# Performance work log

Hardware: AMD Instinct MI355X
Metric: run time of the kernel (lower is better)

The kernel has to match this reference:

```python
import jax, jax.numpy as jnp
import numpy as np

H = 1024  # hidden size

def _gru_layer(x, h0_l, w_ih_l, w_hh_l, b_ih_l, b_hh_l):
    # x: [T,B,I]; precompute input gates for all timesteps (like addmm in the kernel)
    x_gates = jnp.einsum('tbi,gi->tbg', x, w_ih_l) + b_ih_l  # [T,B,3H]

    def step(h, xg):
        # h: [B,H]; xg: [B,3H]
        h_gates = h @ w_hh_l.T + b_hh_l  # [B,3H]
        xr, xz, xn = xg[:, :H], xg[:, H:2*H], xg[:, 2*H:]
        hr, hz, hn = h_gates[:, :H], h_gates[:, H:2*H], h_gates[:, 2*H:]
        r = jax.nn.sigmoid(xr + hr)
        z = jax.nn.sigmoid(xz + hz)
        n = jnp.tanh(xn + r * hn)
        h_new = (1.0 - z) * n + z * h
        return h_new, h_new

    h_final, seq_out = jax.lax.scan(step, h0_l, x_gates)
    return h_final, seq_out


def setup_inputs() -> dict:
    key = jax.random.key(0)
    ks = jax.random.split(key, 6)
    T, B, I, L = 512, 64, 1024, 2
    s = 1.0 / np.sqrt(H)
    return {
        'x': jax.random.normal(ks[0], (T, B, I), dtype=jnp.float32),
        'h0': jax.random.normal(ks[1], (L, B, H), dtype=jnp.float32),
        'w_ih': jax.random.normal(ks[2], (L, 3 * H, I), dtype=jnp.float32) * s,
        'w_hh': jax.random.normal(ks[3], (L, 3 * H, H), dtype=jnp.float32) * s,
        'b_ih': jax.random.normal(ks[4], (L, 3 * H), dtype=jnp.float32) * s,
        'b_hh': jax.random.normal(ks[5], (L, 3 * H), dtype=jnp.float32) * s,
    }


def reference(x, h0, w_ih, w_hh, b_ih, b_hh):
    num_layers = h0.shape[0]
    h_n = []
    cur = x
    for l in range(num_layers):
        h_final, seq_out = _gru_layer(cur, h0[l], w_ih[l], w_hh[l], b_ih[l], b_hh[l])
        h_n.append(h_final)
        cur = seq_out  # layer output becomes next layer's input
    # kernel returns only the final hidden state of every layer, in fp32
    return jnp.stack(h_n, axis=0)  # [L,B,H]
```

## Files before the change

### kernel.cpp

```cpp
#include <hip/hip_runtime.h>

typedef unsigned short u16;
typedef unsigned long long u64;
typedef __attribute__((ext_vector_type(8))) short short8;
typedef __attribute__((ext_vector_type(4))) float f32x4;

#define HH 1024
#define BB 64
#define TT 512
#define G3 3072
#define NBLK 192
#define NS 513
#define SLOT (BB * HH)
#define FSTRIDE 32
#define RING 8

__device__ __forceinline__ u16 f2b(float f) {
  unsigned u = __float_as_uint(f);
  unsigned r = (u + 0x7fffu + ((u >> 16) & 1u)) >> 16;
  return (u16)r;
}
__device__ __forceinline__ float b2f(u16 h) {
  return __uint_as_float(((unsigned)h) << 16);
}
__device__ __forceinline__ float ftanh(float x) {
  x = fminf(15.f, fmaxf(-15.f, x));
  float e = __expf(2.f * x);
  return (e - 1.f) / (e + 1.f);
}

__device__ __forceinline__ void st_u32_agent(unsigned* p, unsigned v) {
  __hip_atomic_store(p, v, __ATOMIC_RELAXED, __HIP_MEMORY_SCOPE_AGENT);
}
__device__ __forceinline__ unsigned ld_u32_agent(const unsigned* p) {
  return __hip_atomic_load(p, __ATOMIC_RELAXED, __HIP_MEMORY_SCOPE_AGENT);
}


__global__ void f32_to_bf16_k(const float* __restrict__ s, u16* __restrict__ d, int n) {
  int stride = gridDim.x * blockDim.x * 4;
  for (int i = (blockIdx.x * blockDim.x + threadIdx.x) * 4; i < n; i += stride) {
    float4 v = *(const float4*)(s + i);
    uint2 p;
    p.x = (unsigned)f2b(v.x) | ((unsigned)f2b(v.y) << 16);
    p.y = (unsigned)f2b(v.z) | ((unsigned)f2b(v.w) << 16);
    *(uint2*)(d + i) = p;
  }
}

__global__ void init_h_k(const float* __restrict__ h0in, u16* __restrict__ hbuf0,
                         u16* __restrict__ hbuf1) {
  int i = blockIdx.x * blockDim.x + threadIdx.x;
  if (i < BB * HH) {
    hbuf0[i] = f2b(h0in[i]);
    hbuf1[i] = f2b(h0in[BB * HH + i]);
  }
}


__global__ __launch_bounds__(256) void gemm_xg_k(
    const u16* __restrict__ A, const u16* __restrict__ Wt,
    const float* __restrict__ bias, u16* __restrict__ C) {
  const int bm = blockIdx.x / 24;
  const int bn = blockIdx.x % 24;
  const int m0 = bm * 128, n0 = bn * 128;
  __shared__ __align__(16) u16 al[128 * 40];
  __shared__ __align__(16) u16 bl[128 * 40];
  const int tid = threadIdx.x;
  const int w = tid >> 6, l = tid & 63;
  const int wr = w >> 1, wc = w & 1;
  const int c0 = tid, c1 = tid + 256;
  const int r0 = c0 >> 2, s0 = c0 & 3, r1 = c1 >> 2, s1 = c1 & 3;

  const f32x4 fzero = {0.f, 0.f, 0.f, 0.f};
  f32x4 acc[4][4];
#pragma unroll
  for (int i = 0; i < 4; ++i)
#pragma unroll
    for (int j = 0; j < 4; ++j) acc[i][j] = fzero;

  const u16* a0p = A + (size_t)(m0 + r0) * 1024 + s0 * 8;
  const u16* a1p = A + (size_t)(m0 + r1) * 1024 + s1 * 8;
  const u16* b0p = Wt + (size_t)(n0 + r0) * 1024 + s0 * 8;
  const u16* b1p = Wt + (size_t)(n0 + r1) * 1024 + s1 * 8;

  int4 va0 = *(const int4*)(a0p);
  int4 va1 = *(const int4*)(a1p);
  int4 vb0 = *(const int4*)(b0p);
  int4 vb1 = *(const int4*)(b1p);

  for (int kt = 0; kt < 32; ++kt) {
    __syncthreads();
    *(int4*)&al[r0 * 40 + s0 * 8] = va0;
    *(int4*)&al[r1 * 40 + s1 * 8] = va1;
    *(int4*)&bl[r0 * 40 + s0 * 8] = vb0;
    *(int4*)&bl[r1 * 40 + s1 * 8] = vb1;
    __syncthreads();
    if (kt < 31) {
      va0 = *(const int4*)(a0p + (kt + 1) * 32);
      va1 = *(const int4*)(a1p + (kt + 1) * 32);
      vb0 = *(const int4*)(b0p + (kt + 1) * 32);
      vb1 = *(const int4*)(b1p + (kt + 1) * 32);
    }
    short8 af[4], bf[4];
#pragma unroll
    for (int i = 0; i < 4; ++i)
      af[i] = *(const short8*)&al[(wr * 64 + i * 16 + (l & 15)) * 40 + (l >> 4) * 8];
#pragma unroll
    for (int j = 0; j < 4; ++j)
      bf[j] = *(const short8*)&bl[(wc * 64 + j * 16 + (l & 15)) * 40 + (l >> 4) * 8];
#pragma unroll
    for (int i = 0; i < 4; ++i)
#pragma unroll
      for (int j = 0; j < 4; ++j)
        acc[i][j] = __builtin_amdgcn_mfma_f32_16x16x32_bf16(af[i], bf[j], acc[i][j], 0, 0, 0);
  }

#pragma unroll
  for (int i = 0; i < 4; ++i) {
#pragma unroll
    for (int j = 0; j < 4; ++j) {
      int col = n0 + wc * 64 + j * 16 + (l & 15);
      float bv = bias[col];
#pragma unroll
      for (int q = 0; q < 4; ++q) {
        int row = m0 + wr * 64 + i * 16 + (l >> 4) * 4 + q;
        C[(size_t)row * G3 + col] = f2b(acc[i][j][q] + bv);
      }
    }
  }
}


__global__ __launch_bounds__(256, 1) void gru_scan11_k(
    const u16* __restrict__ xg0,
    const u16* __restrict__ whh0, const u16* __restrict__ wih1,
    const u16* __restrict__ whh1,
    const float* __restrict__ bhh0, const float* __restrict__ bih1,
    const float* __restrict__ bhh1,
    const float* __restrict__ h0in,
    u16* __restrict__ hbuf0, u16* __restrict__ hbuf1,
    u16* __restrict__ xg1ring, float* __restrict__ out,
    unsigned* __restrict__ flags) {
  const int blk = blockIdx.x;
  const int grp = blk >> 6;
  const int sub = blk & 63;
  const int tid = threadIdx.x;
  const int w = tid >> 6, l = tid & 63;
  const int lrow = l & 15;
  const int kb = (l >> 4) * 8;
  const int myrow0 = w * 16 + (l >> 4) * 4;
  const size_t arow = (size_t)(w * 16 + lrow) * HH + kb;
  const f32x4 fzero = {0.f, 0.f, 0.f, 0.f};

  __shared__ __align__(16) u16 wlds[48 * 1024];
  {
    const u16* Wsrc = (grp == 0) ? whh0 : (grp == 1) ? wih1 : whh1;
    for (int i = tid; i < 6144; i += 256) {
      int r = i >> 7;
      int c = i & 127;
      int g = r >> 4;
      int wrow = g * HH + sub * 16 + (r & 15);
      int4 v = *(const int4*)(Wsrc + (size_t)wrow * 1024 + c * 8);
      int idx = r * 1024 + ((c * 8) ^ ((r & 7) << 3));
      *(int4*)&wlds[idx] = v;
    }
  }
  __syncthreads();
  __builtin_amdgcn_fence(__ATOMIC_ACQUIRE, "agent");

  const int j = sub * 16 + lrow;
  const int sx = (lrow & 7) << 3;

  if (grp == 0) {
    const float bhr = bhh0[j], bhz = bhh0[HH + j], bhn = bhh0[2 * HH + j];
    float hreg[4];
#pragma unroll
    for (int q = 0; q < 4; ++q) hreg[q] = h0in[(myrow0 + q) * HH + j];

    for (int t = 0; t < TT; ++t) {
      u16 xrv[4], xzv[4], xnv[4];
      const u16* xp = xg0 + (size_t)t * BB * G3;
#pragma unroll
      for (int q = 0; q < 4; ++q) {
        const u16* rp = xp + (size_t)(myrow0 + q) * G3;
        xrv[q] = rp[j]; xzv[q] = rp[HH + j]; xnv[q] = rp[2 * HH + j];
      }
      if (t > 0) {
        if (tid < 64) {
          for (;;) {
            unsigned a0 = ld_u32_agent(&flags[l * FSTRIDE]);
            if (__all(a0 >= (unsigned)t)) break;
          }
        }
        __syncthreads();
        __builtin_amdgcn_fence(__ATOMIC_ACQUIRE, "workgroup");
      }

      const u16* Ap = hbuf0 + (size_t)t * SLOT + arow;
      short8 ar[32];
#pragma unroll
      for (int ks = 0; ks < 32; ++ks) ar[ks] = *(const short8*)(Ap + ks * 32);

      f32x4 acc0 = fzero, acc1 = fzero, acc2 = fzero;
#pragma unroll
      for (int ks = 0; ks < 32; ++ks) {
        int ke = kb + ks * 32;
        short8 b0 = *(const short8*)&wlds[(lrow) * 1024 + (ke ^ sx)];
        short8 b1 = *(const short8*)&wlds[(16 + lrow) * 1024 + (ke ^ sx)];
        short8 b2 = *(const short8*)&wlds[(32 + lrow) * 1024 + (ke ^ sx)];
        acc0 = __builtin_amdgcn_mfma_f32_16x16x32_bf16(ar[ks], b0, acc0, 0, 0, 0);
        acc1 = __builtin_amdgcn_mfma_f32_16x16x32_bf16(ar[ks], b1, acc1, 0, 0, 0);
        acc2 = __builtin_amdgcn_mfma_f32_16x16x32_bf16(ar[ks], b2, acc2, 0, 0, 0);
      }

      u16* hbn = hbuf0 + (size_t)(t + 1) * SLOT;
#pragma unroll
      for (int q = 0; q < 4; ++q) {
        float rr = acc0[q] + bhr + b2f(xrv[q]);
        float zz = acc1[q] + bhz + b2f(xzv[q]);
        float nn = acc2[q] + bhn;
        float r = 1.f / (1.f + __expf(-rr));
        float z = 1.f / (1.f + __expf(-zz));
        float n = ftanh(b2f(xnv[q]) + r * nn);
        float hv = (1.f - z) * n + z * hreg[q];
        hreg[q] = hv;
        int hb = (int)f2b(hv);
        int nb = __shfl_xor(hb, 1);
        if ((l & 1) == 0) {
          unsigned pk = (unsigned)(u16)hb | (((unsigned)(u16)nb) << 16);
          st_u32_agent((unsigned*)(hbn + (size_t)(myrow0 + q) * HH + j), pk);
        }
      }

      __syncthreads();
      if (tid == 0) {
        __builtin_amdgcn_fence(__ATOMIC_RELEASE, "workgroup");
        st_u32_agent(&flags[blk * FSTRIDE], (unsigned)(t + 1));
      }
    }
#pragma unroll
    for (int q = 0; q < 4; ++q) out[(size_t)(myrow0 + q) * HH + j] = hreg[q];

  } else if (grp == 1) {
    const float bir = bih1[j], biz = bih1[HH + j], bin = bih1[2 * HH + j];

    for (int t = 1; t <= TT; ++t) {
      if (tid < 64) {
        for (;;) {
          unsigned a0 = ld_u32_agent(&flags[l * FSTRIDE]);
          unsigned a2 = ld_u32_agent(&flags[(128 + l) * FSTRIDE]);
          int ok = (a0 >= (unsigned)t) && ((int)a2 >= t - RING);
          if (__all(ok)) break;
        }
      }
      __syncthreads();
      __builtin_amdgcn_fence(__ATOMIC_ACQUIRE, "workgroup");

      const u16* Ap = hbuf0 + (size_t)t * SLOT + arow;
      short8 ar[32];
#pragma unroll
      for (int ks = 0; ks < 32; ++ks) ar[ks] = *(const short8*)(Ap + ks * 32);

      f32x4 acc0 = fzero, acc1 = fzero, acc2 = fzero;
#pragma unroll
      for (int ks = 0; ks < 32; ++ks) {
        int ke = kb + ks * 32;
        short8 b0 = *(const short8*)&wlds[(lrow) * 1024 + (ke ^ sx)];
        short8 b1 = *(const short8*)&wlds[(16 + lrow) * 1024 + (ke ^ sx)];
        short8 b2 = *(const short8*)&wlds[(32 + lrow) * 1024 + (ke ^ sx)];
        acc0 = __builtin_amdgcn_mfma_f32_16x16x32_bf16(ar[ks], b0, acc0, 0, 0, 0);
        acc1 = __builtin_amdgcn_mfma_f32_16x16x32_bf16(ar[ks], b1, acc1, 0, 0, 0);
        acc2 = __builtin_amdgcn_mfma_f32_16x16x32_bf16(ar[ks], b2, acc2, 0, 0, 0);
      }

      u16* ox = xg1ring + (size_t)(t & (RING - 1)) * (BB * G3);
#pragma unroll
      for (int q = 0; q < 4; ++q) {
        int row = myrow0 + q;
        int a0v = (int)f2b(acc0[q] + bir); int a0n = __shfl_xor(a0v, 1);
        int a1v = (int)f2b(acc1[q] + biz); int a1n = __shfl_xor(a1v, 1);
        int a2v = (int)f2b(acc2[q] + bin); int a2n = __shfl_xor(a2v, 1);
        if ((l & 1) == 0) {
          st_u32_agent((unsigned*)(ox + (size_t)row * G3 + j),
                       (unsigned)(u16)a0v | (((unsigned)(u16)a0n) << 16));
          st_u32_agent((unsigned*)(ox + (size_t)row * G3 + HH + j),
                       (unsigned)(u16)a1v | (((unsigned)(u16)a1n) << 16));
          st_u32_agent((unsigned*)(ox + (size_t)row * G3 + 2 * HH + j),
                       (unsigned)(u16)a2v | (((unsigned)(u16)a2n) << 16));
        }
      }

      __syncthreads();
      if (tid == 0) {
        __builtin_amdgcn_fence(__ATOMIC_RELEASE, "workgroup");
        st_u32_agent(&flags[blk * FSTRIDE], (unsigned)t);
      }
    }

  } else {
    const float bhr = bhh1[j], bhz = bhh1[HH + j], bhn = bhh1[2 * HH + j];
    float hreg[4];
#pragma unroll
    for (int q = 0; q < 4; ++q) hreg[q] = h0in[BB * HH + (myrow0 + q) * HH + j];
    const int jpair = j & ~1;
    const int sel = (j & 1) * 16;

    for (int t = 1; t <= TT; ++t) {
      if (tid < 64) {
        for (;;) {
          unsigned a1 = ld_u32_agent(&flags[(64 + l) * FSTRIDE]);
          unsigned a2 = ld_u32_agent(&flags[(128 + l) * FSTRIDE]);
          int ok = (a1 >= (unsigned)t) && (a2 >= (unsigned)(t - 1));
          if (__all(ok)) break;
        }
      }
      __syncthreads();
      __builtin_amdgcn_fence(__ATOMIC_ACQUIRE, "workgroup");

      const u16* Ap = hbuf1 + (size_t)(t - 1) * SLOT + arow;
      short8 ar[32];
#pragma unroll
      for (int ks = 0; ks < 32; ++ks) ar[ks] = *(const short8*)(Ap + ks * 32);
      const u16* ox = xg1ring + (size_t)(t & (RING - 1)) * (BB * G3);
      float xg1v[3][4];
#pragma unroll
      for (int q = 0; q < 4; ++q) {
        const u16* rp = ox + (size_t)(myrow0 + q) * G3;
        unsigned pr = ld_u32_agent((const unsigned*)(rp + jpair));
        unsigned pz = ld_u32_agent((const unsigned*)(rp + HH + jpair));
        unsigned pn = ld_u32_agent((const unsigned*)(rp + 2 * HH + jpair));
        xg1v[0][q] = b2f((u16)(pr >> sel));
        xg1v[1][q] = b2f((u16)(pz >> sel));
        xg1v[2][q] = b2f((u16)(pn >> sel));
      }

      f32x4 acc0 = fzero, acc1 = fzero, acc2 = fzero;
#pragma unroll
      for (int ks = 0; ks < 32; ++ks) {
        int ke = kb + ks * 32;
        short8 b0 = *(const short8*)&wlds[(lrow) * 1024 + (ke ^ sx)];
        short8 b1 = *(const short8*)&wlds[(16 + lrow) * 1024 + (ke ^ sx)];
        short8 b2 = *(const short8*)&wlds[(32 + lrow) * 1024 + (ke ^ sx)];
        acc0 = __builtin_amdgcn_mfma_f32_16x16x32_bf16(ar[ks], b0, acc0, 0, 0, 0);
        acc1 = __builtin_amdgcn_mfma_f32_16x16x32_bf16(ar[ks], b1, acc1, 0, 0, 0);
        acc2 = __builtin_amdgcn_mfma_f32_16x16x32_bf16(ar[ks], b2, acc2, 0, 0, 0);
      }

      u16* hbn = hbuf1 + (size_t)t * SLOT;
#pragma unroll
      for (int q = 0; q < 4; ++q) {
        float rr = acc0[q] + bhr + xg1v[0][q];
        float zz = acc1[q] + bhz + xg1v[1][q];
        float nn = acc2[q] + bhn;
        float r = 1.f / (1.f + __expf(-rr));
        float z = 1.f / (1.f + __expf(-zz));
        float n = ftanh(xg1v[2][q] + r * nn);
        float hv = (1.f - z) * n + z * hreg[q];
        hreg[q] = hv;
        int hb = (int)f2b(hv);
        int nb = __shfl_xor(hb, 1);
        if ((l & 1) == 0) {
          unsigned pk = (unsigned)(u16)hb | (((unsigned)(u16)nb) << 16);
          st_u32_agent((unsigned*)(hbn + (size_t)(myrow0 + q) * HH + j), pk);
        }
      }

      __syncthreads();
      if (tid == 0) {
        __builtin_amdgcn_fence(__ATOMIC_RELEASE, "workgroup");
        st_u32_agent(&flags[blk * FSTRIDE], (unsigned)t);
      }
    }
#pragma unroll
    for (int q = 0; q < 4; ++q) out[BB * HH + (size_t)(myrow0 + q) * HH + j] = hreg[q];
  }
}


extern "C" void kernel_launch(void* const* d_in, const int* in_sizes, int n_in,
                              void* d_out, int out_size, void* d_ws, size_t ws_size,
                              hipStream_t stream) {
  const float* x   = (const float*)d_in[0];
  const float* h0  = (const float*)d_in[1];
  const float* wih = (const float*)d_in[2];
  const float* whh = (const float*)d_in[3];
  const float* bih = (const float*)d_in[4];
  const float* bhh = (const float*)d_in[5];
  float* out = (float*)d_out;

  char* ws = (char*)d_ws;
  size_t off = 0;
  auto alloc = [&](size_t bytes) -> void* {
    void* p = ws + off;
    off += (bytes + 255) & ~(size_t)255;
    return p;
  };
  u16* xg0   = (u16*)alloc((size_t)TT * BB * G3 * 2);
  u16* wihb  = (u16*)alloc((size_t)2 * G3 * HH * 2);
  u16* whhb  = (u16*)alloc((size_t)2 * G3 * HH * 2);
  size_t hbytes = (size_t)2 * NS * SLOT * 2;
  size_t xbytes = (size_t)TT * BB * HH * 2;
  char* un = (char*)alloc(hbytes > xbytes ? hbytes : xbytes);
  u16* xbf   = (u16*)un;
  u16* hbuf0 = (u16*)un;
  u16* hbuf1 = hbuf0 + (size_t)NS * SLOT;
  u16* xg1ring = (u16*)alloc((size_t)RING * BB * G3 * 2);
  unsigned* flags = (unsigned*)alloc(NBLK * FSTRIDE * 4);

  hipMemsetAsync(flags, 0, NBLK * FSTRIDE * 4, stream);
  f32_to_bf16_k<<<2048, 256, 0, stream>>>(x, xbf, TT * BB * HH);
  f32_to_bf16_k<<<512, 256, 0, stream>>>(wih, wihb, 2 * G3 * HH);
  f32_to_bf16_k<<<512, 256, 0, stream>>>(whh, whhb, 2 * G3 * HH);

  gemm_xg_k<<<6144, 256, 0, stream>>>(xbf, wihb, bih, xg0);

  init_h_k<<<256, 256, 0, stream>>>(h0, hbuf0, hbuf1);

  gru_scan11_k<<<NBLK, 256, 0, stream>>>(xg0,
                                         whhb, wihb + (size_t)G3 * HH, whhb + (size_t)G3 * HH,
                                         bhh, bih + G3, bhh + G3, h0,
                                         hbuf0, hbuf1, xg1ring, out, flags);
}
```

Baseline: 4.419 ms.

## Replace block flag barriers with sentinel-polled hidden state and per-wave flags

Hidden-state buffers are pre-filled with a NaN sentinel. Consumers now poll the hidden-state data directly until no sentinel remains, instead of waiting on global per-block flags with __syncthreads. The handoff between the layer-1 input-projection group and the layer-1 recurrence group uses per-wave flags with an s_waitcnt in place of block barriers and release fences, and the xg1 ring grows from 8 to 32 slots. This is meant to cut cross-block synchronisation latency on the sequential critical path. In exchange it adds a fill kernel over the hidden buffers and relies on relaxed-atomic ordering without explicit release fences, plus the assumption that a real value never equals the sentinel.

```diff
diff --git a/kernel.cpp b/kernel.cpp
--- a/kernel.cpp
+++ b/kernel.cpp
@@ -13,7 +13,8 @@
 #define NS 513
 #define SLOT (BB * HH)
 #define FSTRIDE 32
-#define RING 8
+#define RING 32
+#define SENT 0x7FC07FC0u
 
 __device__ __forceinline__ u16 f2b(float f) {
   unsigned u = __float_as_uint(f);
@@ -34,6 +35,32 @@
 }
 __device__ __forceinline__ unsigned ld_u32_agent(const unsigned* p) {
   return __hip_atomic_load(p, __ATOMIC_RELAXED, __HIP_MEMORY_SCOPE_AGENT);
+}
+__device__ __forceinline__ u64 ld_u64_agent(const u64* p) {
+  return __hip_atomic_load(p, __ATOMIC_RELAXED, __HIP_MEMORY_SCOPE_AGENT);
+}
+
+union AW { short8 s8; u64 d[2]; unsigned w[4]; };
+__device__ __forceinline__ void poll_A(const u16* Ap, AW aw[32]) {
+  const u64* p = (const u64*)Ap;
+#pragma unroll
+  for (int ks = 0; ks < 32; ++ks) {
+    aw[ks].d[0] = ld_u64_agent(p + ks * 8);
+    aw[ks].d[1] = ld_u64_agent(p + ks * 8 + 1);
+  }
+  for (;;) {
+    int bad = 0;
+#pragma unroll
+    for (int ks = 0; ks < 32; ++ks) {
+      if (aw[ks].w[0] == SENT || aw[ks].w[1] == SENT) {
+        aw[ks].d[0] = ld_u64_agent(p + ks * 8); bad = 1;
+      }
+      if (aw[ks].w[2] == SENT || aw[ks].w[3] == SENT) {
+        aw[ks].d[1] = ld_u64_agent(p + ks * 8 + 1); bad = 1;
+      }
+    }
+    if (!bad) break;
+  }
 }
 
 
@@ -46,6 +73,13 @@
     p.y = (unsigned)f2b(v.z) | ((unsigned)f2b(v.w) << 16);
     *(uint2*)(d + i) = p;
   }
+}
+
+__global__ void fill_sent_k(unsigned* __restrict__ d, int n4) {
+  uint4 s = {SENT, SENT, SENT, SENT};
+  int stride = gridDim.x * blockDim.x * 4;
+  for (int i = (blockIdx.x * blockDim.x + threadIdx.x) * 4; i < n4; i += stride)
+    *(uint4*)(d + i) = s;
 }
 
 __global__ void init_h_k(const float* __restrict__ h0in, u16* __restrict__ hbuf0,
@@ -132,7 +166,7 @@
 }
 
 
-__global__ __launch_bounds__(256, 1) void gru_scan11_k(
+__global__ __launch_bounds__(256, 1) void gru_scan12_k(
     const u16* __restrict__ xg0,
     const u16* __restrict__ whh0, const u16* __restrict__ wih1,
     const u16* __restrict__ whh1,
@@ -141,7 +175,7 @@
     const float* __restrict__ h0in,
     u16* __restrict__ hbuf0, u16* __restrict__ hbuf1,
     u16* __restrict__ xg1ring, float* __restrict__ out,
-    unsigned* __restrict__ flags) {
+    unsigned* __restrict__ flags1, unsigned* __restrict__ flags2) {
   const int blk = blockIdx.x;
   const int grp = blk >> 6;
   const int sub = blk & 63;
@@ -167,10 +201,10 @@
     }
   }
   __syncthreads();
-  __builtin_amdgcn_fence(__ATOMIC_ACQUIRE, "agent");
 
   const int j = sub * 16 + lrow;
   const int sx = (lrow & 7) << 3;
+  const int fidx = (sub * 4 + w) * FSTRIDE;
 
   if (grp == 0) {
     const float bhr = bhh0[j], bhz = bhh0[HH + j], bhn = bhh0[2 * HH + j];
@@ -186,21 +220,9 @@
         const u16* rp = xp + (size_t)(myrow0 + q) * G3;
         xrv[q] = rp[j]; xzv[q] = rp[HH + j]; xnv[q] = rp[2 * HH + j];
       }
-      if (t > 0) {
-        if (tid < 64) {
-          for (;;) {
-            unsigned a0 = ld_u32_agent(&flags[l * FSTRIDE]);
-            if (__all(a0 >= (unsigned)t)) break;
-          }
-        }
-        __syncthreads();
-        __builtin_amdgcn_fence(__ATOMIC_ACQUIRE, "workgroup");
-      }
-
-      const u16* Ap = hbuf0 + (size_t)t * SLOT + arow;
-      short8 ar[32];
-#pragma unroll
-      for (int ks = 0; ks < 32; ++ks) ar[ks] = *(const short8*)(Ap + ks * 32);
+
+      AW aw[32];
+      poll_A(hbuf0 + (size_t)t * SLOT + arow, aw);
 
       f32x4 acc0 = fzero, acc1 = fzero, acc2 = fzero;
 #pragma unroll
@@ -209,9 +231,9 @@
         short8 b0 = *(const short8*)&wlds[(lrow) * 1024 + (ke ^ sx)];
         short8 b1 = *(const short8*)&wlds[(16 + lrow) * 1024 + (ke ^ sx)];
         short8 b2 = *(const short8*)&wlds[(32 + lrow) * 1024 + (ke ^ sx)];
-        acc0 = __builtin_amdgcn_mfma_f32_16x16x32_bf16(ar[ks], b0, acc0, 0, 0, 0);
-        acc1 = __builtin_amdgcn_mfma_f32_16x16x32_bf16(ar[ks], b1, acc1, 0, 0, 0);
-        acc2 = __builtin_amdgcn_mfma_f32_16x16x32_bf16(ar[ks], b2, acc2, 0, 0, 0);
+        acc0 = __builtin_amdgcn_mfma_f32_16x16x32_bf16(aw[ks].s8, b0, acc0, 0, 0, 0);
+        acc1 = __builtin_amdgcn_mfma_f32_16x16x32_bf16(aw[ks].s8, b1, acc1, 0, 0, 0);
+        acc2 = __builtin_amdgcn_mfma_f32_16x16x32_bf16(aw[ks].s8, b2, acc2, 0, 0, 0);
       }
 
       u16* hbn = hbuf0 + (size_t)(t + 1) * SLOT;
@@ -232,12 +254,6 @@
           st_u32_agent((unsigned*)(hbn + (size_t)(myrow0 + q) * HH + j), pk);
         }
       }
-
-      __syncthreads();
-      if (tid == 0) {
-        __builtin_amdgcn_fence(__ATOMIC_RELEASE, "workgroup");
-        st_u32_agent(&flags[blk * FSTRIDE], (unsigned)(t + 1));
-      }
     }
 #pragma unroll
     for (int q = 0; q < 4; ++q) out[(size_t)(myrow0 + q) * HH + j] = hreg[q];
@@ -246,21 +262,14 @@
     const float bir = bih1[j], biz = bih1[HH + j], bin = bih1[2 * HH + j];
 
     for (int t = 1; t <= TT; ++t) {
-      if (tid < 64) {
-        for (;;) {
-          unsigned a0 = ld_u32_agent(&flags[l * FSTRIDE]);
-          unsigned a2 = ld_u32_agent(&flags[(128 + l) * FSTRIDE]);
-          int ok = (a0 >= (unsigned)t) && ((int)a2 >= t - RING);
-          if (__all(ok)) break;
-        }
-      }
-      __syncthreads();
+      for (;;) {
+        unsigned f = ld_u32_agent(&flags2[fidx]);
+        if ((int)f >= t - RING) break;
+      }
       __builtin_amdgcn_fence(__ATOMIC_ACQUIRE, "workgroup");
 
-      const u16* Ap = hbuf0 + (size_t)t * SLOT + arow;
-      short8 ar[32];
-#pragma unroll
-      for (int ks = 0; ks < 32; ++ks) ar[ks] = *(const short8*)(Ap + ks * 32);
+      AW aw[32];
+      poll_A(hbuf0 + (size_t)t * SLOT + arow, aw);
 
       f32x4 acc0 = fzero, acc1 = fzero, acc2 = fzero;
 #pragma unroll
@@ -269,9 +278,9 @@
         short8 b0 = *(const short8*)&wlds[(lrow) * 1024 + (ke ^ sx)];
         short8 b1 = *(const short8*)&wlds[(16 + lrow) * 1024 + (ke ^ sx)];
         short8 b2 = *(const short8*)&wlds[(32 + lrow) * 1024 + (ke ^ sx)];
-        acc0 = __builtin_amdgcn_mfma_f32_16x16x32_bf16(ar[ks], b0, acc0, 0, 0, 0);
-        acc1 = __builtin_amdgcn_mfma_f32_16x16x32_bf16(ar[ks], b1, acc1, 0, 0, 0);
-        acc2 = __builtin_amdgcn_mfma_f32_16x16x32_bf16(ar[ks], b2, acc2, 0, 0, 0);
+        acc0 = __builtin_amdgcn_mfma_f32_16x16x32_bf16(aw[ks].s8, b0, acc0, 0, 0, 0);
+        acc1 = __builtin_amdgcn_mfma_f32_16x16x32_bf16(aw[ks].s8, b1, acc1, 0, 0, 0);
+        acc2 = __builtin_amdgcn_mfma_f32_16x16x32_bf16(aw[ks].s8, b2, acc2, 0, 0, 0);
       }
 
       u16* ox = xg1ring + (size_t)(t & (RING - 1)) * (BB * G3);
@@ -290,12 +299,8 @@
                        (unsigned)(u16)a2v | (((unsigned)(u16)a2n) << 16));
         }
       }
-
-      __syncthreads();
-      if (tid == 0) {
-        __builtin_amdgcn_fence(__ATOMIC_RELEASE, "workgroup");
-        st_u32_agent(&flags[blk * FSTRIDE], (unsigned)t);
-      }
+      asm volatile("s_waitcnt vmcnt(0)" ::: "memory");
+      if (l == 0) st_u32_agent(&flags1[fidx], (unsigned)t);
     }
 
   } else {
@@ -307,33 +312,24 @@
     const int sel = (j & 1) * 16;
 
     for (int t = 1; t <= TT; ++t) {
-      if (tid < 64) {
-        for (;;) {
-          unsigned a1 = ld_u32_agent(&flags[(64 + l) * FSTRIDE]);
-          unsigned a2 = ld_u32_agent(&flags[(128 + l) * FSTRIDE]);
-          int ok = (a1 >= (unsigned)t) && (a2 >= (unsigned)(t - 1));
-          if (__all(ok)) break;
-        }
-      }
-      __syncthreads();
+      for (;;) {
+        unsigned f = ld_u32_agent(&flags1[fidx]);
+        if (f >= (unsigned)t) break;
+      }
       __builtin_amdgcn_fence(__ATOMIC_ACQUIRE, "workgroup");
 
-      const u16* Ap = hbuf1 + (size_t)(t - 1) * SLOT + arow;
-      short8 ar[32];
-#pragma unroll
-      for (int ks = 0; ks < 32; ++ks) ar[ks] = *(const short8*)(Ap + ks * 32);
       const u16* ox = xg1ring + (size_t)(t & (RING - 1)) * (BB * G3);
-      float xg1v[3][4];
+      unsigned pr[4], pz[4], pn[4];
 #pragma unroll
       for (int q = 0; q < 4; ++q) {
         const u16* rp = ox + (size_t)(myrow0 + q) * G3;
-        unsigned pr = ld_u32_agent((const unsigned*)(rp + jpair));
-        unsigned pz = ld_u32_agent((const unsigned*)(rp + HH + jpair));
-        unsigned pn = ld_u32_agent((const unsigned*)(rp + 2 * HH + jpair));
-        xg1v[0][q] = b2f((u16)(pr >> sel));
-        xg1v[1][q] = b2f((u16)(pz >> sel));
-        xg1v[2][q] = b2f((u16)(pn >> sel));
-      }
+        pr[q] = ld_u32_agent((const unsigned*)(rp + jpair));
+        pz[q] = ld_u32_agent((const unsigned*)(rp + HH + jpair));
+        pn[q] = ld_u32_agent((const unsigned*)(rp + 2 * HH + jpair));
+      }
+
+      AW aw[32];
+      poll_A(hbuf1 + (size_t)(t - 1) * SLOT + arow, aw);
 
       f32x4 acc0 = fzero, acc1 = fzero, acc2 = fzero;
 #pragma unroll
@@ -342,34 +338,35 @@
         short8 b0 = *(const short8*)&wlds[(lrow) * 1024 + (ke ^ sx)];
         short8 b1 = *(const short8*)&wlds[(16 + lrow) * 1024 + (ke ^ sx)];
         short8 b2 = *(const short8*)&wlds[(32 + lrow) * 1024 + (ke ^ sx)];
-        acc0 = __builtin_amdgcn_mfma_f32_16x16x32_bf16(ar[ks], b0, acc0, 0, 0, 0);
-        acc1 = __builtin_amdgcn_mfma_f32_16x16x32_bf16(ar[ks], b1, acc1, 0, 0, 0);
-        acc2 = __builtin_amdgcn_mfma_f32_16x16x32_bf16(ar[ks], b2, acc2, 0, 0, 0);
-      }
-
-      u16* hbn = hbuf1 + (size_t)t * SLOT;
-#pragma unroll
-      for (int q = 0; q < 4; ++q) {
-        float rr = acc0[q] + bhr + xg1v[0][q];
-        float zz = acc1[q] + bhz + xg1v[1][q];
+        acc0 = __builtin_amdgcn_mfma_f32_16x16x32_bf16(aw[ks].s8, b0, acc0, 0, 0, 0);
+        acc1 = __builtin_amdgcn_mfma_f32_16x16x32_bf16(aw[ks].s8, b1, acc1, 0, 0, 0);
+        acc2 = __builtin_amdgcn_mfma_f32_16x16x32_bf16(aw[ks].s8, b2, acc2, 0, 0, 0);
+      }
+
+      float hv4[4];
+#pragma unroll
+      for (int q = 0; q < 4; ++q) {
+        float rr = acc0[q] + bhr + b2f((u16)(pr[q] >> sel));
+        float zz = acc1[q] + bhz + b2f((u16)(pz[q] >> sel));
         float nn = acc2[q] + bhn;
         float r = 1.f / (1.f + __expf(-rr));
         float z = 1.f / (1.f + __expf(-zz));
-        float n = ftanh(xg1v[2][q] + r * nn);
-        float hv = (1.f - z) * n + z * hreg[q];
-        hreg[q] = hv;
-        int hb = (int)f2b(hv);
+        float n = ftanh(b2f((u16)(pn[q] >> sel)) + r * nn);
+        hv4[q] = (1.f - z) * n + z * hreg[q];
+        hreg[q] = hv4[q];
+      }
+      asm volatile("s_waitcnt vmcnt(0)" ::: "memory");
+      if (l == 0) st_u32_agent(&flags2[fidx], (unsigned)t);
+
+      u16* hbn = hbuf1 + (size_t)t * SLOT;
+#pragma unroll
+      for (int q = 0; q < 4; ++q) {
+        int hb = (int)f2b(hv4[q]);
         int nb = __shfl_xor(hb, 1);
         if ((l & 1) == 0) {
           unsigned pk = (unsigned)(u16)hb | (((unsigned)(u16)nb) << 16);
           st_u32_agent((unsigned*)(hbn + (size_t)(myrow0 + q) * HH + j), pk);
         }
-      }
-
-      __syncthreads();
-      if (tid == 0) {
-        __builtin_amdgcn_fence(__ATOMIC_RELEASE, "workgroup");
-        st_u32_agent(&flags[blk * FSTRIDE], (unsigned)t);
       }
     }
 #pragma unroll
@@ -406,19 +403,22 @@
   u16* hbuf0 = (u16*)un;
   u16* hbuf1 = hbuf0 + (size_t)NS * SLOT;
   u16* xg1ring = (u16*)alloc((size_t)RING * BB * G3 * 2);
-  unsigned* flags = (unsigned*)alloc(NBLK * FSTRIDE * 4);
-
-  hipMemsetAsync(flags, 0, NBLK * FSTRIDE * 4, stream);
+  unsigned* flags1 = (unsigned*)alloc(256 * FSTRIDE * 4);
+  unsigned* flags2 = (unsigned*)alloc(256 * FSTRIDE * 4);
+
+  hipMemsetAsync(flags1, 0, 256 * FSTRIDE * 4, stream);
+  hipMemsetAsync(flags2, 0, 256 * FSTRIDE * 4, stream);
   f32_to_bf16_k<<<2048, 256, 0, stream>>>(x, xbf, TT * BB * HH);
   f32_to_bf16_k<<<512, 256, 0, stream>>>(wih, wihb, 2 * G3 * HH);
   f32_to_bf16_k<<<512, 256, 0, stream>>>(whh, whhb, 2 * G3 * HH);
 
   gemm_xg_k<<<6144, 256, 0, stream>>>(xbf, wihb, bih, xg0);
 
+  fill_sent_k<<<4096, 256, 0, stream>>>((unsigned*)hbuf0, NS * SLOT);
   init_h_k<<<256, 256, 0, stream>>>(h0, hbuf0, hbuf1);
 
-  gru_scan11_k<<<NBLK, 256, 0, stream>>>(xg0,
+  gru_scan12_k<<<NBLK, 256, 0, stream>>>(xg0,
                                          whhb, wihb + (size_t)G3 * HH, whhb + (size_t)G3 * HH,
                                          bhh, bih + G3, bhh + G3, h0,
-                                         hbuf0, hbuf1, xg1ring, out, flags);
-}
+                                         hbuf0, hbuf1, xg1ring, out, flags1, flags2);
+}
```

New measurement: 8.322 ms. 1.88x slower.

## Replace block-level barriers with per-wave flags in the persistent GRU scan

Applied to the files above, without the earlier changes.

Each wave now publishes its own progress flag and waits only on the matching wave (same row slice) in producer blocks, removing the __syncthreads barriers and single-thread flag publishing on every timestep. Layer-1 gate loads from the ring are hoisted ahead of the hidden-state loads, and the ring depth grows from 8 to 32 to loosen producer/consumer coupling. The release ordering now relies on s_waitcnt vmcnt(0) plus relaxed agent-scope stores instead of an explicit release fence. This adds more flag polling traffic and weaker memory-ordering guarantees.

```diff
diff --git a/kernel.cpp b/kernel.cpp
--- a/kernel.cpp
+++ b/kernel.cpp
@@ -13,7 +13,7 @@
 #define NS 513
 #define SLOT (BB * HH)
 #define FSTRIDE 32
-#define RING 8
+#define RING 32
 
 __device__ __forceinline__ u16 f2b(float f) {
   unsigned u = __float_as_uint(f);
@@ -132,7 +132,7 @@
 }
 
 
-__global__ __launch_bounds__(256, 1) void gru_scan11_k(
+__global__ __launch_bounds__(256, 1) void gru_scan13_k(
     const u16* __restrict__ xg0,
     const u16* __restrict__ whh0, const u16* __restrict__ wih1,
     const u16* __restrict__ whh1,
@@ -141,7 +141,8 @@
     const float* __restrict__ h0in,
     u16* __restrict__ hbuf0, u16* __restrict__ hbuf1,
     u16* __restrict__ xg1ring, float* __restrict__ out,
-    unsigned* __restrict__ flags) {
+    unsigned* __restrict__ flags0, unsigned* __restrict__ flags1,
+    unsigned* __restrict__ flags2) {
   const int blk = blockIdx.x;
   const int grp = blk >> 6;
   const int sub = blk & 63;
@@ -171,6 +172,8 @@
 
   const int j = sub * 16 + lrow;
   const int sx = (lrow & 7) << 3;
+  const int myf = (sub * 4 + w) * FSTRIDE;
+  const int plf = (l * 4 + w) * FSTRIDE;
 
   if (grp == 0) {
     const float bhr = bhh0[j], bhz = bhh0[HH + j], bhn = bhh0[2 * HH + j];
@@ -187,15 +190,12 @@
         xrv[q] = rp[j]; xzv[q] = rp[HH + j]; xnv[q] = rp[2 * HH + j];
       }
       if (t > 0) {
-        if (tid < 64) {
-          for (;;) {
-            unsigned a0 = ld_u32_agent(&flags[l * FSTRIDE]);
-            if (__all(a0 >= (unsigned)t)) break;
-          }
+        for (;;) {
+          unsigned a0 = ld_u32_agent(&flags0[plf]);
+          if (__all(a0 >= (unsigned)t)) break;
         }
-        __syncthreads();
-        __builtin_amdgcn_fence(__ATOMIC_ACQUIRE, "workgroup");
-      }
+      }
+      __builtin_amdgcn_fence(__ATOMIC_ACQUIRE, "workgroup");
 
       const u16* Ap = hbuf0 + (size_t)t * SLOT + arow;
       short8 ar[32];
@@ -232,12 +232,8 @@
           st_u32_agent((unsigned*)(hbn + (size_t)(myrow0 + q) * HH + j), pk);
         }
       }
-
-      __syncthreads();
-      if (tid == 0) {
-        __builtin_amdgcn_fence(__ATOMIC_RELEASE, "workgroup");
-        st_u32_agent(&flags[blk * FSTRIDE], (unsigned)(t + 1));
-      }
+      asm volatile("s_waitcnt vmcnt(0)" ::: "memory");
+      if (l == 0) st_u32_agent(&flags0[myf], (unsigned)(t + 1));
     }
 #pragma unroll
     for (int q = 0; q < 4; ++q) out[(size_t)(myrow0 + q) * HH + j] = hreg[q];
@@ -246,15 +242,12 @@
     const float bir = bih1[j], biz = bih1[HH + j], bin = bih1[2 * HH + j];
 
     for (int t = 1; t <= TT; ++t) {
-      if (tid < 64) {
-        for (;;) {
-          unsigned a0 = ld_u32_agent(&flags[l * FSTRIDE]);
-          unsigned a2 = ld_u32_agent(&flags[(128 + l) * FSTRIDE]);
-          int ok = (a0 >= (unsigned)t) && ((int)a2 >= t - RING);
-          if (__all(ok)) break;
-        }
-      }
-      __syncthreads();
+      for (;;) {
+        unsigned a0 = ld_u32_agent(&flags0[plf]);
+        unsigned f2 = ld_u32_agent(&flags2[myf]);
+        int ok = (a0 >= (unsigned)t) && ((int)f2 >= t - RING);
+        if (__all(ok)) break;
+      }
       __builtin_amdgcn_fence(__ATOMIC_ACQUIRE, "workgroup");
 
       const u16* Ap = hbuf0 + (size_t)t * SLOT + arow;
@@ -290,12 +283,8 @@
                        (unsigned)(u16)a2v | (((unsigned)(u16)a2n) << 16));
         }
       }
-
-      __syncthreads();
-      if (tid == 0) {
-        __builtin_amdgcn_fence(__ATOMIC_RELEASE, "workgroup");
-        st_u32_agent(&flags[blk * FSTRIDE], (unsigned)t);
-      }
+      asm volatile("s_waitcnt vmcnt(0)" ::: "memory");
+      if (l == 0) st_u32_agent(&flags1[myf], (unsigned)t);
     }
 
   } else {
@@ -307,33 +296,27 @@
     const int sel = (j & 1) * 16;
 
     for (int t = 1; t <= TT; ++t) {
-      if (tid < 64) {
-        for (;;) {
-          unsigned a1 = ld_u32_agent(&flags[(64 + l) * FSTRIDE]);
-          unsigned a2 = ld_u32_agent(&flags[(128 + l) * FSTRIDE]);
-          int ok = (a1 >= (unsigned)t) && (a2 >= (unsigned)(t - 1));
-          if (__all(ok)) break;
-        }
-      }
-      __syncthreads();
+      for (;;) {
+        unsigned f1 = ld_u32_agent(&flags1[myf]);
+        unsigned a2 = ld_u32_agent(&flags2[plf]);
+        int ok = (f1 >= (unsigned)t) && (a2 >= (unsigned)(t - 1));
+        if (__all(ok)) break;
+      }
       __builtin_amdgcn_fence(__ATOMIC_ACQUIRE, "workgroup");
 
+      const u16* ox = xg1ring + (size_t)(t & (RING - 1)) * (BB * G3);
+      unsigned pr[4], pz[4], pn[4];
+#pragma unroll
+      for (int q = 0; q < 4; ++q) {
+        const u16* rp = ox + (size_t)(myrow0 + q) * G3;
+        pr[q] = ld_u32_agent((const unsigned*)(rp + jpair));
+        pz[q] = ld_u32_agent((const unsigned*)(rp + HH + jpair));
+        pn[q] = ld_u32_agent((const unsigned*)(rp + 2 * HH + jpair));
+      }
       const u16* Ap = hbuf1 + (size_t)(t - 1) * SLOT + arow;
       short8 ar[32];
 #pragma unroll
       for (int ks = 0; ks < 32; ++ks) ar[ks] = *(const short8*)(Ap + ks * 32);
-      const u16* ox = xg1ring + (size_t)(t & (RING - 1)) * (BB * G3);
-      float xg1v[3][4];
-#pragma unroll
-      for (int q = 0; q < 4; ++q) {
-        const u16* rp = ox + (size_t)(myrow0 + q) * G3;
-        unsigned pr = ld_u32_agent((const unsigned*)(rp + jpair));
-        unsigned pz = ld_u32_agent((const unsigned*)(rp + HH + jpair));
-        unsigned pn = ld_u32_agent((const unsigned*)(rp + 2 * HH + jpair));
-        xg1v[0][q] = b2f((u16)(pr >> sel));
-        xg1v[1][q] = b2f((u16)(pz >> sel));
-        xg1v[2][q] = b2f((u16)(pn >> sel));
-      }
 
       f32x4 acc0 = fzero, acc1 = fzero, acc2 = fzero;
 #pragma unroll
@@ -350,12 +333,12 @@
       u16* hbn = hbuf1 + (size_t)t * SLOT;
 #pragma unroll
       for (int q = 0; q < 4; ++q) {
-        float rr = acc0[q] + bhr + xg1v[0][q];
-        float zz = acc1[q] + bhz + xg1v[1][q];
+        float rr = acc0[q] + bhr + b2f((u16)(pr[q] >> sel));
+        float zz = acc1[q] + bhz + b2f((u16)(pz[q] >> sel));
         float nn = acc2[q] + bhn;
         float r = 1.f / (1.f + __expf(-rr));
         float z = 1.f / (1.f + __expf(-zz));
-        float n = ftanh(xg1v[2][q] + r * nn);
+        float n = ftanh(b2f((u16)(pn[q] >> sel)) + r * nn);
         float hv = (1.f - z) * n + z * hreg[q];
         hreg[q] = hv;
         int hb = (int)f2b(hv);
@@ -365,12 +348,8 @@
           st_u32_agent((unsigned*)(hbn + (size_t)(myrow0 + q) * HH + j), pk);
         }
       }
-
-      __syncthreads();
-      if (tid == 0) {
-        __builtin_amdgcn_fence(__ATOMIC_RELEASE, "workgroup");
-        st_u32_agent(&flags[blk * FSTRIDE], (unsigned)t);
-      }
+      asm volatile("s_waitcnt vmcnt(0)" ::: "memory");
+      if (l == 0) st_u32_agent(&flags2[myf], (unsigned)t);
     }
 #pragma unroll
     for (int q = 0; q < 4; ++q) out[BB * HH + (size_t)(myrow0 + q) * HH + j] = hreg[q];
@@ -406,9 +385,13 @@
   u16* hbuf0 = (u16*)un;
   u16* hbuf1 = hbuf0 + (size_t)NS * SLOT;
   u16* xg1ring = (u16*)alloc((size_t)RING * BB * G3 * 2);
-  unsigned* flags = (unsigned*)alloc(NBLK * FSTRIDE * 4);
-
-  hipMemsetAsync(flags, 0, NBLK * FSTRIDE * 4, stream);
+  unsigned* flags0 = (unsigned*)alloc(256 * FSTRIDE * 4);
+  unsigned* flags1 = (unsigned*)alloc(256 * FSTRIDE * 4);
+  unsigned* flags2 = (unsigned*)alloc(256 * FSTRIDE * 4);
+
+  hipMemsetAsync(flags0, 0, 256 * FSTRIDE * 4, stream);
+  hipMemsetAsync(flags1, 0, 256 * FSTRIDE * 4, stream);
+  hipMemsetAsync(flags2, 0, 256 * FSTRIDE * 4, stream);
   f32_to_bf16_k<<<2048, 256, 0, stream>>>(x, xbf, TT * BB * HH);
   f32_to_bf16_k<<<512, 256, 0, stream>>>(wih, wihb, 2 * G3 * HH);
   f32_to_bf16_k<<<512, 256, 0, stream>>>(whh, whhb, 2 * G3 * HH);
@@ -417,8 +400,9 @@
 
   init_h_k<<<256, 256, 0, stream>>>(h0, hbuf0, hbuf1);
 
-  gru_scan11_k<<<NBLK, 256, 0, stream>>>(xg0,
+  gru_scan13_k<<<NBLK, 256, 0, stream>>>(xg0,
                                          whhb, wihb + (size_t)G3 * HH, whhb + (size_t)G3 * HH,
                                          bhh, bih + G3, bhh + G3, h0,
-                                         hbuf0, hbuf1, xg1ring, out, flags);
-}
+                                         hbuf0, hbuf1, xg1ring, out,
+                                         flags0, flags1, flags2);
+}
```

Result: slower. 5.391 ms (+22.0%).
